# Performance work log

Hardware: AMD Instinct MI355X
Metric: run time of the kernel (lower is better)

The kernel has to match this reference:

```python
import jax, jax.numpy as jnp
import numpy as np


def _gru_dir(x, mask, W, U, b, reverse):
    """Keras GRU (reset_after=True) over time with masking.

    x: [B, S, D] float, mask: [B, S] bool, W: [D, 3U], U: [U, 3U], b: [2, 3U].
    Gate order z, r, h. Masked steps carry the previous state/output.
    reverse=True == Keras go_backwards + re-reversed outputs.
    """
    B, S, D = x.shape
    units = U.shape[0]
    b_in, b_rec = b[0], b[1]

    def step(h, inp):
        xt, mt = inp  # xt: [B, D], mt: [B]
        gx = xt @ W + b_in          # [B, 3U]
        gh = h @ U + b_rec          # [B, 3U]
        xz, xr, xh = jnp.split(gx, 3, axis=-1)
        rz, rr, rh = jnp.split(gh, 3, axis=-1)
        z = jax.nn.sigmoid(xz + rz)
        r = jax.nn.sigmoid(xr + rr)
        hh = jnp.tanh(xh + r * rh)
        hn = z * h + (1.0 - z) * hh
        hn = jnp.where(mt[:, None], hn, h)  # masked step: carry state
        return hn, hn

    xs = jnp.swapaxes(x, 0, 1)      # [S, B, D]
    ms = jnp.swapaxes(mask, 0, 1)   # [S, B]
    h0 = jnp.zeros((B, units), x.dtype)
    _, outs = jax.lax.scan(step, h0, (xs, ms), reverse=reverse)
    return jnp.swapaxes(outs, 0, 1)  # [B, S, U]


def setup_inputs() -> dict:
    key = jax.random.key(0)
    ks = jax.random.split(key, 8)
    B, S, V, U = 64, 512, 32000, 256
    x = jax.random.randint(ks[0], (B, S), 0, V, dtype=jnp.int64)
    s = 0.05
    return {
        "x": x,
        "emb": jax.random.normal(ks[1], (V, U), jnp.float32) * s,
        "Wf": jax.random.normal(ks[2], (U, 3 * U), jnp.float32) * s,
        "Uf": jax.random.normal(ks[3], (U, 3 * U), jnp.float32) * s,
        "bf": jax.random.normal(ks[4], (2, 3 * U), jnp.float32) * s,
        "Wb": jax.random.normal(ks[5], (U, 3 * U), jnp.float32) * s,
        "Ub": jax.random.normal(ks[6], (U, 3 * U), jnp.float32) * s,
        "bb": jax.random.normal(ks[7], (2, 3 * U), jnp.float32) * s,
    }


def reference(x, emb, Wf, Uf, bf, Wb, Ub, bb):
    mask = x != 0                 # Embedding(mask_zero=True)
    e = emb[x]                    # [B, S, U]
    fwd = _gru_dir(e, mask, Wf, Uf, bf, reverse=False)
    bwd = _gru_dir(e, mask, Wb, Ub, bb, reverse=True)
    return fwd + bwd              # Bidirectional(merge_mode='sum')
```

## Files before the change

kernel.cpp:

```cpp
#include <hip/hip_runtime.h>
#include <hip/hip_bf16.h>


typedef short short8 __attribute__((ext_vector_type(8)));
typedef float f32x4 __attribute__((ext_vector_type(4)));

__device__ __forceinline__ unsigned short f2bf(float f) {
  unsigned int u = __float_as_uint(f);
  return (unsigned short)((u + 0x7fffu + ((u >> 16) & 1u)) >> 16);
}
__device__ __forceinline__ float blo(unsigned int u) { return __uint_as_float(u << 16); }
__device__ __forceinline__ float bhi(unsigned int u) { return __uint_as_float(u & 0xffff0000u); }
__device__ __forceinline__ float sigf(float x) {
  return __builtin_amdgcn_rcpf(1.f + __expf(-x));
}
__device__ __forceinline__ float tanhfast(float x) {
  return 1.f - 2.f * __builtin_amdgcn_rcpf(1.f + __expf(2.f * x));
}
__device__ __forceinline__ void lds_barrier() {
  __builtin_amdgcn_sched_barrier(0);
  asm volatile("s_waitcnt lgkmcnt(0)" ::: "memory");
  __builtin_amdgcn_s_barrier();
  __builtin_amdgcn_sched_barrier(0);
}

__global__ void __launch_bounds__(256) wt_prep_kernel(const float* __restrict__ Wf,
                                                      const float* __restrict__ Wb,
                                                      unsigned short* __restrict__ Wtb) {
  int o = blockIdx.x * 256 + threadIdx.x;
  if (o >= 2 * 768 * 256) return;
  int dir = o / (768 * 256);
  int rem = o % (768 * 256);
  int c = rem / 256, k = rem % 256;
  const float* W = dir ? Wb : Wf;
  Wtb[o] = f2bf(W[(size_t)k * 768 + c]);
}

__global__ void __launch_bounds__(256) u_prep_kernel(const float* __restrict__ Uf,
                                                     const float* __restrict__ Ub,
                                                     unsigned short* __restrict__ Upk) {
  int id = blockIdx.x * 256 + threadIdx.x;
  if (id >= 2 * 8 * 6 * 8 * 64) return;
  int lane = id & 63;
  int kk = (id >> 6) & 7;
  int s = (id >> 9) % 6;
  int w = (id / 3072) & 7;
  int dir = id / 24576;
  const float* U = dir ? Ub : Uf;
  int g = s >> 1, d = s & 1;
  int gcol = g * 256 + w * 32 + d * 16 + (lane & 15);
  int k0 = kk * 32 + (lane >> 4) * 8;
  unsigned short* o = Upk + (size_t)id * 8;
#pragma unroll
  for (int e = 0; e < 8; ++e) o[e] = f2bf(U[(size_t)(k0 + e) * 768 + gcol]);
}

__global__ void __launch_bounds__(256) gx_mfma_kernel(
    const int* __restrict__ x, const float* __restrict__ emb,
    const unsigned short* __restrict__ Wtb,
    const float* __restrict__ bfv, const float* __restrict__ bbv,
    unsigned short* __restrict__ gx4) {
  __shared__ __align__(16) unsigned short As[128 * 32];
  __shared__ __align__(16) unsigned short Bs[128 * 32];
  __shared__ int xid[128];

  int tid = threadIdx.x;
  int r0 = blockIdx.x * 128;
  int yt = blockIdx.y;
  int dir = (yt >= 6) ? 1 : 0;
  int c0 = (yt - dir * 6) * 128;
  const float* bv = dir ? bbv : bfv;
  const unsigned short* WtD = Wtb + (size_t)dir * 768 * 256;

  if (tid < 128) xid[tid] = x[r0 + tid];
  __syncthreads();

  int lane = tid & 63, w = tid >> 6;
  int wr = w >> 1, wc = w & 1;

  f32x4 acc[4][4] = {};

  for (int ks = 0; ks < 8; ++ks) {
#pragma unroll
    for (int i = 0; i < 2; ++i) {
      int s = tid + i * 256;
      int row = s >> 2, kslot = s & 3;
      int sw = kslot ^ ((row >> 2) & 3);
      const float* src = emb + (size_t)xid[row] * 256 + ks * 32 + kslot * 8;
      float4 f0 = *(const float4*)src;
      float4 f1 = *(const float4*)(src + 4);
      uint4 pa;
      pa.x = f2bf(f0.x) | ((unsigned)f2bf(f0.y) << 16);
      pa.y = f2bf(f0.z) | ((unsigned)f2bf(f0.w) << 16);
      pa.z = f2bf(f1.x) | ((unsigned)f2bf(f1.y) << 16);
      pa.w = f2bf(f1.z) | ((unsigned)f2bf(f1.w) << 16);
      *(uint4*)&As[row * 32 + sw * 8] = pa;
      uint4 pb = *(const uint4*)(WtD + (size_t)(c0 + row) * 256 + ks * 32 + kslot * 8);
      *(uint4*)&Bs[row * 32 + sw * 8] = pb;
    }
    __syncthreads();

    short8 a[4], b[4];
#pragma unroll
    for (int f = 0; f < 4; ++f) {
      int rowA = wr * 64 + f * 16 + (lane & 15);
      int swA = (lane >> 4) ^ ((rowA >> 2) & 3);
      a[f] = __builtin_bit_cast(short8, *(const uint4*)&As[rowA * 32 + swA * 8]);
      int rowB = wc * 64 + f * 16 + (lane & 15);
      int swB = (lane >> 4) ^ ((rowB >> 2) & 3);
      b[f] = __builtin_bit_cast(short8, *(const uint4*)&Bs[rowB * 32 + swB * 8]);
    }
#pragma unroll
    for (int fm = 0; fm < 4; ++fm)
#pragma unroll
      for (int fn = 0; fn < 4; ++fn)
        acc[fm][fn] = __builtin_amdgcn_mfma_f32_16x16x32_bf16(a[fm], b[fn], acc[fm][fn], 0, 0, 0);
    __syncthreads();
  }

#pragma unroll
  for (int fn = 0; fn < 4; ++fn) {
    int col = c0 + wc * 64 + fn * 16 + (lane & 15);
    float bias = bv[col] + (col < 512 ? bv[768 + col] : 0.f);
    int g = col >> 8, u = col & 255;
    int w2 = u >> 5, d = (u >> 4) & 1, cl2 = u & 15;
#pragma unroll
    for (int fm = 0; fm < 4; ++fm) {
      int rowb = r0 + wr * 64 + fm * 16 + (lane >> 4) * 4;
#pragma unroll
      for (int q = 0; q < 4; ++q) {
        int row = rowb + q;
        int bb2 = row >> 9, tt2 = row & 511;
        int G = bb2 & 3, bg2 = bb2 >> 2;
        size_t idx = ((size_t)(dir * 512 + tt2) * 3 + g) * 16384
                     + (size_t)((bg2 * 8 + w2) * 64 + (G * 16 + cl2)) * 2 + d;
        gx4[idx] = f2bf(acc[fm][fn][q] + bias);
      }
    }
  }
}

__global__ void __launch_bounds__(512, 1) gru_kernel(
    const unsigned short* __restrict__ Upk,
    const unsigned short* __restrict__ gx4,
    const int* __restrict__ x,
    const float* __restrict__ bfv, const float* __restrict__ bbv,
    float* __restrict__ out) {
  int wg = blockIdx.x;
  int dir = wg >> 4, bg = wg & 15;
  int tid = threadIdx.x;
  int w = tid >> 6, l = tid & 63;
  int G = l >> 4, cl = l & 15;
  int b = bg * 4 + G;

  __shared__ __align__(16) unsigned short h_lds[2][4096];

  short8 Ufr[6][8];
  {
    const unsigned short* ub = Upk + (size_t)(dir * 8 + w) * 24576 + (size_t)l * 8;
#pragma unroll
    for (int s = 0; s < 6; ++s)
#pragma unroll
      for (int kk = 0; kk < 8; ++kk)
        Ufr[s][kk] = __builtin_bit_cast(short8, *(const uint4*)(ub + (s * 8 + kk) * 512));
  }

  {
    uint4 z = {0u, 0u, 0u, 0u};
    ((uint4*)h_lds)[tid] = z;
    ((uint4*)h_lds)[512 + tid] = z;
  }

  const float* bv = dir ? bbv : bfv;
  float brh[2];
#pragma unroll
  for (int d = 0; d < 2; ++d) brh[d] = bv[1280 + w * 32 + d * 16 + cl];
  float* outb = out + ((size_t)b << 17);

  int amask = (cl & 7) << 4;
  float h_old[2] = {0.f, 0.f};

  int t0 = dir ? 511 : 0;
  long sdelta = dir ? -98304 : 98304;
  const char* gp = (const char*)gx4 + ((size_t)(dir * 512 + t0) * 98304)
                   + (size_t)((bg * 8 + w) * 64 + l) * 4;
  const int* xp = x + b * 512 + t0;
  int xdelta = dir ? -1 : 1;

  unsigned int gq0 = *(const unsigned int*)(gp);
  unsigned int gq1 = *(const unsigned int*)(gp + 32768);
  unsigned int gq2 = *(const unsigned int*)(gp + 65536);
  int xv = *xp;
  __syncthreads();

  int cur = 0;
  int tcur = t0;
  for (int step = 0; step < 512; ++step) {
    const char* gpn = (step < 511) ? gp + sdelta : gp;
    const int* xpn = (step < 511) ? xp + xdelta : xp;
    unsigned int gn0 = *(const unsigned int*)(gpn);
    unsigned int gn1 = *(const unsigned int*)(gpn + 32768);
    unsigned int gn2 = *(const unsigned int*)(gpn + 65536);
    int xn = *xpn;

    f32x4 acc[6];
#pragma unroll
    for (int s = 0; s < 6; ++s) acc[s] = (f32x4){0.f, 0.f, 0.f, 0.f};
    const char* hb = (const char*)(&h_lds[cur][0]);
#pragma unroll
    for (int kk = 0; kk < 8; ++kk) {
      short8 a = __builtin_bit_cast(short8,
          *(const uint4*)(hb + cl * 512 + (((kk << 6) | (G << 4)) ^ amask)));
#pragma unroll
      for (int s = 0; s < 6; ++s)
        acc[s] = __builtin_amdgcn_mfma_f32_16x16x32_bf16(a, Ufr[s][kk], acc[s], 0, 0, 0);
    }

    char* hw = (char*)(&h_lds[cur ^ 1][0]);
#pragma unroll
    for (int d = 0; d < 2; ++d) {
      float gz = d ? bhi(gq0) : blo(gq0);
      float gr = d ? bhi(gq1) : blo(gq1);
      float gh = d ? bhi(gq2) : blo(gq2);
      float z = sigf(gz + acc[0 + d][0]);
      float r = sigf(gr + acc[2 + d][0]);
      float hh = tanhfast(gh + r * (acc[4 + d][0] + brh[d]));
      float hn = hh + z * (h_old[d] - hh);
      hn = (xv == 0) ? h_old[d] : hn;
      h_old[d] = hn;
      int u = w * 32 + d * 16 + cl;
      *(unsigned short*)(hw + G * 2048 + ((u * 2) ^ ((G & 1) << 6))) = f2bf(hn);
      atomicAdd(&outb[(size_t)tcur * 256 + u], hn);
    }
    lds_barrier();
    gq0 = gn0; gq1 = gn1; gq2 = gn2; xv = xn;
    gp = gpn; xp = xpn;
    tcur += (step < 511) ? xdelta : 0;
    cur ^= 1;
  }
}

extern "C" void kernel_launch(void* const* d_in, const int* in_sizes, int n_in,
                              void* d_out, int out_size, void* d_ws, size_t ws_size,
                              hipStream_t stream) {
  const int*   x   = (const int*)d_in[0];
  const float* emb = (const float*)d_in[1];
  const float* Wf  = (const float*)d_in[2];
  const float* Uf  = (const float*)d_in[3];
  const float* bf_ = (const float*)d_in[4];
  const float* Wb  = (const float*)d_in[5];
  const float* Ub  = (const float*)d_in[6];
  const float* bb_ = (const float*)d_in[7];
  float* out = (float*)d_out;

  unsigned short* gx4 = (unsigned short*)d_ws;
  unsigned short* Wtb = (unsigned short*)((char*)d_ws + 100663296);
  unsigned short* Upk = (unsigned short*)((char*)d_ws + 100663296 + 786432);

  hipMemsetAsync(d_out, 0, (size_t)out_size * sizeof(float), stream);

  wt_prep_kernel<<<1536, 256, 0, stream>>>(Wf, Wb, Wtb);
  u_prep_kernel<<<192, 256, 0, stream>>>(Uf, Ub, Upk);
  gx_mfma_kernel<<<dim3(256, 12), 256, 0, stream>>>(x, emb, Wtb, bf_, bb_, gx4);
  gru_kernel<<<32, 512, 0, stream>>>(Upk, gx4, x, bf_, bb_, out);
}
```

Before: 607.4 us.

## Split GRU recurrence across 16 waves per block with one column tile each

Doubles the recurrent kernel's workgroup from 512 to 1024 threads. Each wave now owns 16 hidden units instead of 32, so it holds half the recurrent weight fragments and issues half the MFMAs per timestep. The packed U layout, the gx4 layout and the per-step gate loads are reworked to match one unit per lane. The intent is to shorten the serial per-step critical path by spreading MFMA work across more waves. In exchange, each block barrier now synchronises twice as many waves.

```diff
diff --git a/kernel.cpp b/kernel.cpp
--- a/kernel.cpp
+++ b/kernel.cpp
@@ -9,8 +9,9 @@
   unsigned int u = __float_as_uint(f);
   return (unsigned short)((u + 0x7fffu + ((u >> 16) & 1u)) >> 16);
 }
-__device__ __forceinline__ float blo(unsigned int u) { return __uint_as_float(u << 16); }
-__device__ __forceinline__ float bhi(unsigned int u) { return __uint_as_float(u & 0xffff0000u); }
+__device__ __forceinline__ float bf2f(unsigned short v) {
+  return __uint_as_float((unsigned int)v << 16);
+}
 __device__ __forceinline__ float sigf(float x) {
   return __builtin_amdgcn_rcpf(1.f + __expf(-x));
 }
@@ -40,15 +41,14 @@
                                                      const float* __restrict__ Ub,
                                                      unsigned short* __restrict__ Upk) {
   int id = blockIdx.x * 256 + threadIdx.x;
-  if (id >= 2 * 8 * 6 * 8 * 64) return;
+  if (id >= 2 * 16 * 3 * 8 * 64) return;
   int lane = id & 63;
   int kk = (id >> 6) & 7;
-  int s = (id >> 9) % 6;
-  int w = (id / 3072) & 7;
+  int s = (id >> 9) % 3;
+  int w = (id / 1536) & 15;
   int dir = id / 24576;
   const float* U = dir ? Ub : Uf;
-  int g = s >> 1, d = s & 1;
-  int gcol = g * 256 + w * 32 + d * 16 + (lane & 15);
+  int gcol = s * 256 + w * 16 + (lane & 15);
   int k0 = kk * 32 + (lane >> 4) * 8;
   unsigned short* o = Upk + (size_t)id * 8;
 #pragma unroll
@@ -123,7 +123,7 @@
     int col = c0 + wc * 64 + fn * 16 + (lane & 15);
     float bias = bv[col] + (col < 512 ? bv[768 + col] : 0.f);
     int g = col >> 8, u = col & 255;
-    int w2 = u >> 5, d = (u >> 4) & 1, cl2 = u & 15;
+    int w2 = (u >> 4) & 15, cl2 = u & 15;
 #pragma unroll
     for (int fm = 0; fm < 4; ++fm) {
       int rowb = r0 + wr * 64 + fm * 16 + (lane >> 4) * 4;
@@ -133,14 +133,14 @@
         int bb2 = row >> 9, tt2 = row & 511;
         int G = bb2 & 3, bg2 = bb2 >> 2;
         size_t idx = ((size_t)(dir * 512 + tt2) * 3 + g) * 16384
-                     + (size_t)((bg2 * 8 + w2) * 64 + (G * 16 + cl2)) * 2 + d;
+                     + (size_t)((bg2 * 16 + w2) * 64 + (G * 16 + cl2));
         gx4[idx] = f2bf(acc[fm][fn][q] + bias);
       }
     }
   }
 }
 
-__global__ void __launch_bounds__(512, 1) gru_kernel(
+__global__ void __launch_bounds__(1024, 1) gru_kernel(
     const unsigned short* __restrict__ Upk,
     const unsigned short* __restrict__ gx4,
     const int* __restrict__ x,
@@ -152,14 +152,15 @@
   int w = tid >> 6, l = tid & 63;
   int G = l >> 4, cl = l & 15;
   int b = bg * 4 + G;
+  int u = w * 16 + cl;
 
   __shared__ __align__(16) unsigned short h_lds[2][4096];
 
-  short8 Ufr[6][8];
+  short8 Ufr[3][8];
   {
-    const unsigned short* ub = Upk + (size_t)(dir * 8 + w) * 24576 + (size_t)l * 8;
-#pragma unroll
-    for (int s = 0; s < 6; ++s)
+    const unsigned short* ub = Upk + (size_t)(dir * 16 + w) * 12288 + (size_t)l * 8;
+#pragma unroll
+    for (int s = 0; s < 3; ++s)
 #pragma unroll
       for (int kk = 0; kk < 8; ++kk)
         Ufr[s][kk] = __builtin_bit_cast(short8, *(const uint4*)(ub + (s * 8 + kk) * 512));
@@ -168,74 +169,70 @@
   {
     uint4 z = {0u, 0u, 0u, 0u};
     ((uint4*)h_lds)[tid] = z;
-    ((uint4*)h_lds)[512 + tid] = z;
   }
 
   const float* bv = dir ? bbv : bfv;
-  float brh[2];
-#pragma unroll
-  for (int d = 0; d < 2; ++d) brh[d] = bv[1280 + w * 32 + d * 16 + cl];
-  float* outb = out + ((size_t)b << 17);
+  const float brh = bv[1280 + u];
+  float* outp;
+  {
+    int t0i = dir ? 511 : 0;
+    outp = out + ((size_t)b << 17) + (size_t)t0i * 256 + u;
+  }
+  long odelta = (dir ? -256 : 256) * (long)sizeof(float);
 
   int amask = (cl & 7) << 4;
-  float h_old[2] = {0.f, 0.f};
+  float h_old = 0.f;
 
   int t0 = dir ? 511 : 0;
   long sdelta = dir ? -98304 : 98304;
   const char* gp = (const char*)gx4 + ((size_t)(dir * 512 + t0) * 98304)
-                   + (size_t)((bg * 8 + w) * 64 + l) * 4;
+                   + (size_t)((bg * 16 + w) * 64 + l) * 2;
   const int* xp = x + b * 512 + t0;
   int xdelta = dir ? -1 : 1;
 
-  unsigned int gq0 = *(const unsigned int*)(gp);
-  unsigned int gq1 = *(const unsigned int*)(gp + 32768);
-  unsigned int gq2 = *(const unsigned int*)(gp + 65536);
+  float gz = bf2f(*(const unsigned short*)(gp));
+  float gr = bf2f(*(const unsigned short*)(gp + 32768));
+  float gh = bf2f(*(const unsigned short*)(gp + 65536));
   int xv = *xp;
   __syncthreads();
 
   int cur = 0;
-  int tcur = t0;
   for (int step = 0; step < 512; ++step) {
     const char* gpn = (step < 511) ? gp + sdelta : gp;
     const int* xpn = (step < 511) ? xp + xdelta : xp;
-    unsigned int gn0 = *(const unsigned int*)(gpn);
-    unsigned int gn1 = *(const unsigned int*)(gpn + 32768);
-    unsigned int gn2 = *(const unsigned int*)(gpn + 65536);
+    float gzn = bf2f(*(const unsigned short*)(gpn));
+    float grn = bf2f(*(const unsigned short*)(gpn + 32768));
+    float ghn = bf2f(*(const unsigned short*)(gpn + 65536));
     int xn = *xpn;
 
-    f32x4 acc[6];
-#pragma unroll
-    for (int s = 0; s < 6; ++s) acc[s] = (f32x4){0.f, 0.f, 0.f, 0.f};
+    f32x4 acc[3];
+#pragma unroll
+    for (int s = 0; s < 3; ++s) acc[s] = (f32x4){0.f, 0.f, 0.f, 0.f};
     const char* hb = (const char*)(&h_lds[cur][0]);
 #pragma unroll
     for (int kk = 0; kk < 8; ++kk) {
       short8 a = __builtin_bit_cast(short8,
           *(const uint4*)(hb + cl * 512 + (((kk << 6) | (G << 4)) ^ amask)));
 #pragma unroll
-      for (int s = 0; s < 6; ++s)
+      for (int s = 0; s < 3; ++s)
         acc[s] = __builtin_amdgcn_mfma_f32_16x16x32_bf16(a, Ufr[s][kk], acc[s], 0, 0, 0);
     }
 
     char* hw = (char*)(&h_lds[cur ^ 1][0]);
-#pragma unroll
-    for (int d = 0; d < 2; ++d) {
-      float gz = d ? bhi(gq0) : blo(gq0);
-      float gr = d ? bhi(gq1) : blo(gq1);
-      float gh = d ? bhi(gq2) : blo(gq2);
-      float z = sigf(gz + acc[0 + d][0]);
-      float r = sigf(gr + acc[2 + d][0]);
-      float hh = tanhfast(gh + r * (acc[4 + d][0] + brh[d]));
-      float hn = hh + z * (h_old[d] - hh);
-      hn = (xv == 0) ? h_old[d] : hn;
-      h_old[d] = hn;
-      int u = w * 32 + d * 16 + cl;
+    {
+      float z = sigf(gz + acc[0][0]);
+      float r = sigf(gr + acc[1][0]);
+      float hh = tanhfast(gh + r * (acc[2][0] + brh));
+      float hn = hh + z * (h_old - hh);
+      hn = (xv == 0) ? h_old : hn;
+      h_old = hn;
       *(unsigned short*)(hw + G * 2048 + ((u * 2) ^ ((G & 1) << 6))) = f2bf(hn);
-      atomicAdd(&outb[(size_t)tcur * 256 + u], hn);
+      atomicAdd(outp, hn);
     }
     lds_barrier();
-    gq0 = gn0; gq1 = gn1; gq2 = gn2; xv = xn;
+    gz = gzn; gr = grn; gh = ghn; xv = xn;
     gp = gpn; xp = xpn;
-    tcur += (step < 511) ? xdelta : 0;
+    if (step < 511) outp = (float*)((char*)outp + odelta);
     cur ^= 1;
   }
 }
@@ -262,5 +259,5 @@
   wt_prep_kernel<<<1536, 256, 0, stream>>>(Wf, Wb, Wtb);
   u_prep_kernel<<<192, 256, 0, stream>>>(Uf, Ub, Upk);
   gx_mfma_kernel<<<dim3(256, 12), 256, 0, stream>>>(x, emb, Wtb, bf_, bb_, gx4);
-  gru_kernel<<<32, 512, 0, stream>>>(Upk, gx4, x, bf_, bb_, out);
-}
+  gru_kernel<<<32, 1024, 0, stream>>>(Upk, gx4, x, bf_, bb_, out);
+}
```

After: 983.0 us. +61.9%, slower.
